# Performance work log

Measured on AMD Instinct MI355X. Metric: run time of the kernel, lower is better.

## Reference

```python
import jax, jax.numpy as jnp
import numpy as np

NUM_USERS = 100000
NUM_ITEMS = 50000
NUM_EDGES = 2000000
DIM = 64
NUM_REL = 5


def setup_inputs() -> dict:
    key = jax.random.key(0)
    k1, k2, k3, k4, k5, k6 = jax.random.split(key, 6)
    u_features = jax.random.normal(k1, (NUM_USERS, DIM), dtype=jnp.float32)
    i_features = jax.random.normal(k2, (NUM_ITEMS, DIM), dtype=jnp.float32)
    edge_user = jax.random.randint(k3, (NUM_EDGES,), 0, NUM_USERS, dtype=jnp.int64)
    edge_item = jax.random.randint(k4, (NUM_EDGES,), 0, NUM_ITEMS, dtype=jnp.int64)
    # per-relation Linear params, torch convention: y = x @ W[r].T + b[r]
    W = jax.random.normal(k5, (NUM_REL, DIM, DIM), dtype=jnp.float32) * (1.0 / np.sqrt(DIM))
    b = jax.random.normal(k6, (NUM_REL, DIM), dtype=jnp.float32) * 0.01
    return {"u_features": u_features, "i_features": i_features,
            "edge_user": edge_user, "edge_item": edge_item, "W": W, "b": b}


def reference(u_features, i_features, edge_user, edge_item, W, b):
    # gather edge endpoint features: [E, D]
    edge_u = u_features[edge_user]
    edge_i = i_features[edge_item]
    num_rel = W.shape[0]
    # per relation: sum((edge_u @ W[r].T + b[r]) * edge_i, axis=1) -> [E]
    # loop over small fixed relation count to avoid [E, R, D] intermediate
    cols = [jnp.sum((edge_u @ W[r].T + b[r]) * edge_i, axis=1)
            for r in range(num_rel)]
    return jnp.stack(cols, axis=1)  # [E, R]
```

## Files before the change

kernel.cpp:

```cpp
#include <hip/hip_runtime.h>
#include <stdint.h>

#define NREL 5
#define D 64
#define Q_BYTES 320
#define NT 21
#define NB 8
#define CHUNK 4096
#define EDGE_GRID 2048

typedef __attribute__((ext_vector_type(8))) short short8;
typedef __attribute__((ext_vector_type(4))) float f32x4;

static __device__ __forceinline__ short f2bf(float f) {
    uint32_t u = __float_as_uint(f);
    u += 0x7FFFu + ((u >> 16) & 1u);
    return (short)(u >> 16);
}

#if defined(__has_builtin)
#if __has_builtin(__builtin_amdgcn_sdot4)
#define HAVE_SDOT4 1
#endif
#endif
#ifdef HAVE_SDOT4
static __device__ __forceinline__ int SDOT4(uint32_t a, uint32_t b, int c) {
    return __builtin_amdgcn_sdot4((int)a, (int)b, c, false);
}
#else
static __device__ __forceinline__ int SDOT4(uint32_t a, uint32_t b, int c) {
    c += ((int)(a << 24) >> 24) * ((int)(b << 24) >> 24);
    c += ((int)(a << 16) >> 24) * ((int)(b << 16) >> 24);
    c += ((int)(a << 8) >> 24) * ((int)(b << 8) >> 24);
    c += ((int)a >> 24) * ((int)b >> 24);
    return c;
}
#endif

__global__ __launch_bounds__(256) void prep_kernel(
    const float* __restrict__ W, const float* __restrict__ bias_p, short* __restrict__ Wf,
    const float* __restrict__ uf, uint32_t* __restrict__ uq, float* __restrict__ uscale,
    int nUsers,
    const int* __restrict__ edge_user, const int* __restrict__ edge_item,
    int nE, int bucketDiv, int cap,
    int* __restrict__ totals, unsigned long long* __restrict__ sorted)
{
    __shared__ int cnt[NB];
    __shared__ int base[NB];
    const int nbW = (NT * 2 * 64 + 255) / 256;
    const int nbU = (nUsers * 16 + 255) / 256;
    int bid = blockIdx.x;

    if (bid < nbW) {
        const int tid = bid * 256 + threadIdx.x;
        if (tid >= NT * 2 * 64) return;
        const int lane = tid & 63;
        const int h = (tid >> 6) & 1;
        const int nt = tid >> 7;
        const int ln = lane & 15, quad = lane >> 4;
        const int n = nt * 16 + ln;
        uint32_t w[4];
#pragma unroll
        for (int p = 0; p < 4; ++p) {
            uint32_t lo = 0, hi = 0;
#pragma unroll
            for (int s = 0; s < 2; ++s) {
                const int j = p * 2 + s;
                const int d = h * 32 + quad * 8 + j;
                float v;
                if (nt < 20) v = W[(n >> 6) * (D * D) + d * D + (n & 63)];
                else         v = (ln < NREL) ? bias_p[ln * D + d] : 0.f;
                if (s == 0) lo = (uint16_t)f2bf(v); else hi = (uint16_t)f2bf(v);
            }
            w[p] = lo | (hi << 16);
        }
        *(uint4*)(Wf + (size_t)tid * 8) = make_uint4(w[0], w[1], w[2], w[3]);
        return;
    }
    bid -= nbW;

    if (bid < nbU) {
        const int gid = bid * 256 + threadIdx.x;
        const int row = gid >> 4;
        const int t = gid & 15;
        if (row >= nUsers) return;
        const float* rp = uf + (size_t)row * D;
        const float v0 = rp[t], v1 = rp[16 + t], v2 = rp[32 + t], v3 = rp[48 + t];
        float m = fmaxf(fmaxf(fabsf(v0), fabsf(v1)), fmaxf(fabsf(v2), fabsf(v3)));
        m = fmaxf(m, __shfl_xor(m, 1));
        m = fmaxf(m, __shfl_xor(m, 2));
        m = fmaxf(m, __shfl_xor(m, 4));
        m = fmaxf(m, __shfl_xor(m, 8));
        m = fmaxf(m, 1e-20f);
        const float qs = 127.0f / m;
        const int q0 = (int)rintf(v0 * qs);
        const int q1 = (int)rintf(v1 * qs);
        const int q2 = (int)rintf(v2 * qs);
        const int q3 = (int)rintf(v3 * qs);
        uq[(size_t)row * 16 + t] = ((uint32_t)(uint8_t)(int8_t)q0)
                                 | ((uint32_t)(uint8_t)(int8_t)q1 << 8)
                                 | ((uint32_t)(uint8_t)(int8_t)q2 << 16)
                                 | ((uint32_t)(uint8_t)(int8_t)q3 << 24);
        if (t == 0) uscale[row] = m * (1.0f / 127.0f);
        return;
    }
    bid -= nbU;

    if (threadIdx.x < NB) cnt[threadIdx.x] = 0;
    __syncthreads();

    const long start = (long)bid * CHUNK;
    unsigned long long pk[CHUNK / 256];
    unsigned long long bins = 0;
    unsigned long long accLo = 0, accHi = 0;
#pragma unroll
    for (int k = 0; k < CHUNK / 256; ++k) {
        const long e = start + k * 256 + threadIdx.x;
        const bool ok = (e < nE);
        int iu = 0, ii = 0;
        if (ok) { iu = edge_user[e]; ii = edge_item[e]; }
        pk[k] = ok ? ((unsigned long long)(uint32_t)iu
                    | ((unsigned long long)(uint32_t)ii << 17)
                    | ((unsigned long long)e << 33))
                   : ~0ull;
        const int bn = ok ? (ii / bucketDiv) : 0;
        bins |= (unsigned long long)bn << (k * 3);
        if (ok) {
            const unsigned long long one = 1ull << ((bn & 3) * 16);
            if (bn < 4) accLo += one; else accHi += one;
        }
    }
#pragma unroll
    for (int d = 1; d < 64; d <<= 1) {
        accLo += __shfl_xor(accLo, d);
        accHi += __shfl_xor(accHi, d);
    }
    if ((threadIdx.x & 63) == 0) {
#pragma unroll
        for (int f = 0; f < 4; ++f) {
            atomicAdd(&cnt[f],     (int)((accLo >> (f * 16)) & 0xFFFF));
            atomicAdd(&cnt[4 + f], (int)((accHi >> (f * 16)) & 0xFFFF));
        }
    }
    __syncthreads();
    if (threadIdx.x < NB) {
        const int c = cnt[threadIdx.x];
        base[threadIdx.x] = threadIdx.x * cap + atomicAdd(&totals[threadIdx.x], c);
        cnt[threadIdx.x] = 0;
    }
    __syncthreads();
#pragma unroll
    for (int k = 0; k < CHUNK / 256; ++k) {
        if (pk[k] != ~0ull) {
            const int bn = (int)((bins >> (k * 3)) & 7);
            const int r = atomicAdd(&cnt[bn], 1);
            sorted[base[bn] + r] = pk[k];
        }
    }
}

__global__ __launch_bounds__(256) void item_transform_kernel(
    const float* __restrict__ i_feat,
    const short* __restrict__ Wf,
    char* __restrict__ qrecs,
    float* __restrict__ sc,
    int nItems)
{
    const int lane = threadIdx.x & 63;
    const int wv = threadIdx.x >> 6;
    const int m0 = blockIdx.x * 64 + wv * 16;
    const int ln = lane & 15, quad = lane >> 4;

    int rowA = m0 + ln;
    if (rowA >= nItems) rowA = nItems - 1;
    const float* ap = i_feat + (size_t)rowA * D + quad * 8;
    short8 af[2];
#pragma unroll
    for (int h = 0; h < 2; ++h) {
        const float4 x = *(const float4*)(ap + h * 32);
        const float4 y = *(const float4*)(ap + h * 32 + 4);
        short8 a;
        a[0] = f2bf(x.x); a[1] = f2bf(x.y); a[2] = f2bf(x.z); a[3] = f2bf(x.w);
        a[4] = f2bf(y.x); a[5] = f2bf(y.y); a[6] = f2bf(y.z); a[7] = f2bf(y.w);
        af[h] = a;
    }

    f32x4 acc[NT];
#pragma unroll
    for (int nt = 0; nt < NT; ++nt) acc[nt] = (f32x4){0.f, 0.f, 0.f, 0.f};

#pragma unroll
    for (int nt = 0; nt < NT; ++nt) {
        const short8 b0 = *(const short8*)(Wf + ((size_t)(nt * 2 + 0) * 64 + lane) * 8);
        acc[nt] = __builtin_amdgcn_mfma_f32_16x16x32_bf16(af[0], b0, acc[nt], 0, 0, 0);
        const short8 b1 = *(const short8*)(Wf + ((size_t)(nt * 2 + 1) * 64 + lane) * 8);
        acc[nt] = __builtin_amdgcn_mfma_f32_16x16x32_bf16(af[1], b1, acc[nt], 0, 0, 0);
    }

#pragma unroll
    for (int g = 0; g < 4; ++g) {
        const int item = m0 + quad * 4 + g;
        const bool ok = (item < nItems);
        char* rec = qrecs + (size_t)item * Q_BYTES;
#pragma unroll
        for (int r = 0; r < NREL; ++r) {
            const float v0 = acc[4 * r + 0][g];
            const float v1 = acc[4 * r + 1][g];
            const float v2 = acc[4 * r + 2][g];
            const float v3 = acc[4 * r + 3][g];
            float m = fmaxf(fmaxf(fabsf(v0), fabsf(v1)), fmaxf(fabsf(v2), fabsf(v3)));
            m = fmaxf(m, __shfl_xor(m, 1));
            m = fmaxf(m, __shfl_xor(m, 2));
            m = fmaxf(m, __shfl_xor(m, 4));
            m = fmaxf(m, __shfl_xor(m, 8));
            m = fmaxf(m, 1e-20f);
            const float qs = 127.0f / m;
            const uint32_t pw = ((uint32_t)(uint8_t)(int8_t)(int)rintf(v0 * qs))
                              | ((uint32_t)(uint8_t)(int8_t)(int)rintf(v1 * qs) << 8)
                              | ((uint32_t)(uint8_t)(int8_t)(int)rintf(v2 * qs) << 16)
                              | ((uint32_t)(uint8_t)(int8_t)(int)rintf(v3 * qs) << 24);
            if (ok) {
                *(uint32_t*)(rec + r * D + ln * 4) = pw;
                if (ln == 0) sc[(size_t)item * 16 + 2 * r] = m * (1.0f / 127.0f);
            }
        }
        if (ok && ln < NREL) sc[(size_t)item * 16 + 2 * ln + 1] = acc[20][g];
    }
}

__global__ __launch_bounds__(256) void edge_kernel(
    const uint32_t* __restrict__ u_q,
    const float* __restrict__ u_scale,
    const unsigned long long* __restrict__ sorted,
    const int* __restrict__ totals, int cap,
    const char* __restrict__ qrecs,
    const float* __restrict__ sc,
    float* __restrict__ out)
{
    const int b = blockIdx.x & 7;
    const int seg = blockIdx.x >> 3;
    const int nSeg = gridDim.x >> 3;
    const int s0 = b * cap;
    const int s1 = s0 + totals[b];
    const int cnt = s1 - s0;
    const int per = (cnt + nSeg - 1) / nSeg;
    const int p0 = s0 + seg * per;
    const int p1 = min(p0 + per, s1);

    const int lane = threadIdx.x & 63;
    const int wv = threadIdx.x >> 6;
    const int es = lane >> 2;
    const int c = lane & 3;

    for (int q0 = p0 + wv * 16; q0 < p1; q0 += 64) {
        const int pos = q0 + es;
        if (pos < p1) {
            const unsigned long long pk = sorted[pos];
            const int iu = (int)(pk & 0x1FFFF);
            const int ii = (int)((pk >> 17) & 0xFFFF);
            const long e = (long)(pk >> 33);

            const uint4 uv = *(const uint4*)(u_q + (size_t)iu * 16 + c * 4);
            const char* rec = qrecs + (size_t)ii * Q_BYTES;

            int s[NREL];
#pragma unroll
            for (int r = 0; r < NREL; ++r) {
                const uint4 yv = *(const uint4*)(rec + r * D + c * 16);
                int t = SDOT4(uv.x, yv.x, 0);
                t = SDOT4(uv.y, yv.y, t);
                t = SDOT4(uv.z, yv.z, t);
                s[r] = SDOT4(uv.w, yv.w, t);
            }
#pragma unroll
            for (int r = 0; r < NREL; ++r) {
                s[r] += __shfl_xor(s[r], 1);
                s[r] += __shfl_xor(s[r], 2);
            }
            const float us = u_scale[iu];
            const float* scp = sc + (size_t)ii * 16;
            const float2 sb = *(const float2*)(scp + 2 * c);
            out[e * NREL + c] = fmaf((float)s[c], us * sb.x, sb.y);
            if (c == 0) {
                const float2 sb4 = *(const float2*)(scp + 8);
                out[e * NREL + 4] = fmaf((float)s[4], us * sb4.x, sb4.y);
            }
        }
    }
}

extern "C" void kernel_launch(void* const* d_in, const int* in_sizes, int n_in,
                              void* d_out, int out_size, void* d_ws, size_t ws_size,
                              hipStream_t stream) {
    const float* u_feat    = (const float*)d_in[0];
    const float* i_feat    = (const float*)d_in[1];
    const int*   edge_user = (const int*)d_in[2];
    const int*   edge_item = (const int*)d_in[3];
    const float* W         = (const float*)d_in[4];
    const float* b         = (const float*)d_in[5];
    float* out = (float*)d_out;

    const int nUsers = in_sizes[0] / D;
    const int nItems = in_sizes[1] / D;
    const int nE = in_sizes[2];
    const int bucketDiv = (nItems + NB - 1) / NB;
    const int nBlocksSort = (nE + CHUNK - 1) / CHUNK;
    const int cap = nE / NB + 32768;

    size_t off = 0;
    char* qrecs = (char*)d_ws;
    off += ((size_t)nItems * Q_BYTES + 255) & ~(size_t)255;
    float* sc = (float*)((char*)d_ws + off);
    off += ((size_t)nItems * 16 * sizeof(float) + 255) & ~(size_t)255;
    uint32_t* u_q = (uint32_t*)((char*)d_ws + off);
    off += ((size_t)nUsers * D + 255) & ~(size_t)255;
    float* u_scale = (float*)((char*)d_ws + off);
    off += ((size_t)nUsers * sizeof(float) + 255) & ~(size_t)255;
    short* Wf = (short*)((char*)d_ws + off);
    off += ((size_t)NT * 2 * 64 * 8 * sizeof(short) + 255) & ~(size_t)255;
    int* totals = (int*)((char*)d_ws + off);
    off += 256;
    unsigned long long* sorted = (unsigned long long*)((char*)d_ws + off);

    hipMemsetAsync(totals, 0, NB * sizeof(int), stream);

    const int nbW = (NT * 2 * 64 + 255) / 256;
    const int nbU = (nUsers * 16 + 255) / 256;
    prep_kernel<<<nbW + nbU + nBlocksSort, 256, 0, stream>>>(
        W, b, Wf, u_feat, u_q, u_scale, nUsers,
        edge_user, edge_item, nE, bucketDiv, cap, totals, sorted);
    item_transform_kernel<<<(nItems + 63) / 64, 256, 0, stream>>>(i_feat, Wf, qrecs, sc, nItems);
    edge_kernel<<<EDGE_GRID, 256, 0, stream>>>(u_q, u_scale, sorted, totals, cap,
                                               qrecs, sc, out);
}
```

Measured before the change: 259.1 us.

## Write edge results in sorted order, then unpermute to output order

The edge kernel now writes its per-edge results contiguously in bucket-sorted order with nontemporal stores, instead of scattering them to random output rows. The sort kernel also records a permutation, and a new unperm kernel gathers the results back to edge order with coalesced output writes. This is meant to cut the cost of scattered partial-line writes, at the price of an extra kernel launch, extra intermediate traffic (perm, resA, resB), and a dependence on workspace size. The bucket capacity slack is also reduced, which risks overflowing a bucket if bin counts are skewed.

```diff
diff --git a/kernel.cpp b/kernel.cpp
--- a/kernel.cpp
+++ b/kernel.cpp
@@ -43,7 +43,8 @@
     int nUsers,
     const int* __restrict__ edge_user, const int* __restrict__ edge_item,
     int nE, int bucketDiv, int cap,
-    int* __restrict__ totals, unsigned long long* __restrict__ sorted)
+    int* __restrict__ totals, unsigned long long* __restrict__ sorted,
+    int* __restrict__ perm, int twoPass)
 {
     __shared__ int cnt[NB];
     __shared__ int base[NB];
@@ -152,9 +153,12 @@
 #pragma unroll
     for (int k = 0; k < CHUNK / 256; ++k) {
         if (pk[k] != ~0ull) {
+            const long e = start + k * 256 + threadIdx.x;
             const int bn = (int)((bins >> (k * 3)) & 7);
             const int r = atomicAdd(&cnt[bn], 1);
-            sorted[base[bn] + r] = pk[k];
+            const int pos = base[bn] + r;
+            sorted[pos] = pk[k];
+            if (twoPass) perm[e] = pos;
         }
     }
 }
@@ -235,7 +239,10 @@
     const int* __restrict__ totals, int cap,
     const char* __restrict__ qrecs,
     const float* __restrict__ sc,
-    float* __restrict__ out)
+    float* __restrict__ resA,
+    float* __restrict__ resB,
+    float* __restrict__ out,
+    int twoPass)
 {
     const int b = blockIdx.x & 7;
     const int seg = blockIdx.x >> 3;
@@ -258,7 +265,6 @@
             const unsigned long long pk = sorted[pos];
             const int iu = (int)(pk & 0x1FFFF);
             const int ii = (int)((pk >> 17) & 0xFFFF);
-            const long e = (long)(pk >> 33);
 
             const uint4 uv = *(const uint4*)(u_q + (size_t)iu * 16 + c * 4);
             const char* rec = qrecs + (size_t)ii * Q_BYTES;
@@ -280,11 +286,41 @@
             const float us = u_scale[iu];
             const float* scp = sc + (size_t)ii * 16;
             const float2 sb = *(const float2*)(scp + 2 * c);
-            out[e * NREL + c] = fmaf((float)s[c], us * sb.x, sb.y);
+            const float v_c = fmaf((float)s[c], us * sb.x, sb.y);
+            float v_4 = 0.f;
             if (c == 0) {
                 const float2 sb4 = *(const float2*)(scp + 8);
-                out[e * NREL + 4] = fmaf((float)s[4], us * sb4.x, sb4.y);
-            }
+                v_4 = fmaf((float)s[4], us * sb4.x, sb4.y);
+            }
+            if (twoPass) {
+                __builtin_nontemporal_store(v_c, resA + (size_t)pos * 4 + c);
+                if (c == 0) __builtin_nontemporal_store(v_4, resB + pos);
+            } else {
+                const long e = (long)(pk >> 33);
+                out[e * NREL + c] = v_c;
+                if (c == 0) out[e * NREL + 4] = v_4;
+            }
+        }
+    }
+}
+
+__global__ __launch_bounds__(256) void unperm_kernel(
+    const int* __restrict__ perm,
+    const float4* __restrict__ resA,
+    const float* __restrict__ resB,
+    int nE,
+    float* __restrict__ out)
+{
+    const long start = (long)blockIdx.x * CHUNK;
+#pragma unroll
+    for (int k = 0; k < CHUNK / 256; ++k) {
+        const long e = start + k * 256 + threadIdx.x;
+        if (e < nE) {
+            const int p = perm[e];
+            const float4 a = resA[p];
+            const float b5 = resB[p];
+            float* op = out + e * NREL;
+            op[0] = a.x; op[1] = a.y; op[2] = a.z; op[3] = a.w; op[4] = b5;
         }
     }
 }
@@ -305,7 +341,7 @@
     const int nE = in_sizes[2];
     const int bucketDiv = (nItems + NB - 1) / NB;
     const int nBlocksSort = (nE + CHUNK - 1) / CHUNK;
-    const int cap = nE / NB + 32768;
+    const int cap = nE / NB + 4096;
 
     size_t off = 0;
     char* qrecs = (char*)d_ws;
@@ -321,6 +357,14 @@
     int* totals = (int*)((char*)d_ws + off);
     off += 256;
     unsigned long long* sorted = (unsigned long long*)((char*)d_ws + off);
+    off += ((size_t)NB * cap * sizeof(unsigned long long) + 255) & ~(size_t)255;
+    int* perm = (int*)((char*)d_ws + off);
+    size_t off2 = off + (((size_t)nE * sizeof(int) + 255) & ~(size_t)255);
+    float* resA = (float*)((char*)d_ws + off2);
+    off2 += ((size_t)NB * cap * 4 * sizeof(float) + 255) & ~(size_t)255;
+    float* resB = (float*)((char*)d_ws + off2);
+    off2 += ((size_t)NB * cap * sizeof(float) + 255) & ~(size_t)255;
+    const int twoPass = (ws_size >= off2) ? 1 : 0;
 
     hipMemsetAsync(totals, 0, NB * sizeof(int), stream);
 
@@ -328,8 +372,10 @@
     const int nbU = (nUsers * 16 + 255) / 256;
     prep_kernel<<<nbW + nbU + nBlocksSort, 256, 0, stream>>>(
         W, b, Wf, u_feat, u_q, u_scale, nUsers,
-        edge_user, edge_item, nE, bucketDiv, cap, totals, sorted);
+        edge_user, edge_item, nE, bucketDiv, cap, totals, sorted, perm, twoPass);
     item_transform_kernel<<<(nItems + 63) / 64, 256, 0, stream>>>(i_feat, Wf, qrecs, sc, nItems);
     edge_kernel<<<EDGE_GRID, 256, 0, stream>>>(u_q, u_scale, sorted, totals, cap,
-                                               qrecs, sc, out);
-}
+                                               qrecs, sc, resA, resB, out, twoPass);
+    if (twoPass)
+        unperm_kernel<<<nBlocksSort, 256, 0, stream>>>(perm, (const float4*)resA, resB, nE, out);
+}
```

New measurement: 258.6 us. No clear change (-0.2%).

## Compact sort keys, write sorted-order results, and unpermute outputs in separate pass

Applied to the files above, without the earlier changes.

The sort records shrink from 64-bit to 32-bit by storing the bucket-local item index and dropping the edge id. A 16-bit per-edge permutation and per-block bucket bases are recorded instead. The edge kernel now writes results contiguously in sorted order with nontemporal stores, replacing scattered 20-byte output writes, and a new unperm kernel gathers them back into edge order. Item transform is merged into the user-quant/sort kernel, while W prep moves to its own tiny kernel. The cost is an extra kernel launch plus extra intermediate read/write traffic, and the bucket slack is reduced.

```diff
diff --git a/kernel.cpp b/kernel.cpp
--- a/kernel.cpp
+++ b/kernel.cpp
@@ -37,205 +37,206 @@
 }
 #endif
 
-__global__ __launch_bounds__(256) void prep_kernel(
-    const float* __restrict__ W, const float* __restrict__ bias_p, short* __restrict__ Wf,
-    const float* __restrict__ uf, uint32_t* __restrict__ uq, float* __restrict__ uscale,
-    int nUsers,
+__global__ __launch_bounds__(256) void wprep_kernel(
+    const float* __restrict__ W, const float* __restrict__ bias_p, short* __restrict__ Wf)
+{
+    const int tid = blockIdx.x * 256 + threadIdx.x;
+    if (tid >= NT * 2 * 64) return;
+    const int lane = tid & 63;
+    const int h = (tid >> 6) & 1;
+    const int nt = tid >> 7;
+    const int ln = lane & 15, quad = lane >> 4;
+    const int n = nt * 16 + ln;
+    uint32_t w[4];
+#pragma unroll
+    for (int p = 0; p < 4; ++p) {
+        uint32_t lo = 0, hi = 0;
+#pragma unroll
+        for (int s = 0; s < 2; ++s) {
+            const int j = p * 2 + s;
+            const int d = h * 32 + quad * 8 + j;
+            float v;
+            if (nt < 20) v = W[(n >> 6) * (D * D) + d * D + (n & 63)];
+            else         v = (ln < NREL) ? bias_p[ln * D + d] : 0.f;
+            if (s == 0) lo = (uint16_t)f2bf(v); else hi = (uint16_t)f2bf(v);
+        }
+        w[p] = lo | (hi << 16);
+    }
+    *(uint4*)(Wf + (size_t)tid * 8) = make_uint4(w[0], w[1], w[2], w[3]);
+}
+
+__global__ __launch_bounds__(256) void fused_kernel(
+    const float* __restrict__ i_feat, const short* __restrict__ Wf,
+    char* __restrict__ qrecs, float* __restrict__ sc, int nItems,
+    const float* __restrict__ uf, uint32_t* __restrict__ uq,
+    float* __restrict__ uscale, int nUsers,
     const int* __restrict__ edge_user, const int* __restrict__ edge_item,
     int nE, int bucketDiv, int cap,
-    int* __restrict__ totals, unsigned long long* __restrict__ sorted)
+    int* __restrict__ totals, uint32_t* __restrict__ sorted,
+    uint16_t* __restrict__ perm, int* __restrict__ blockBase)
 {
     __shared__ int cnt[NB];
     __shared__ int base[NB];
-    const int nbW = (NT * 2 * 64 + 255) / 256;
-    const int nbU = (nUsers * 16 + 255) / 256;
+    const int nbI = (nItems + 63) / 64;
+    const int nbS = (nE + CHUNK - 1) / CHUNK;
     int bid = blockIdx.x;
 
-    if (bid < nbW) {
-        const int tid = bid * 256 + threadIdx.x;
-        if (tid >= NT * 2 * 64) return;
-        const int lane = tid & 63;
-        const int h = (tid >> 6) & 1;
-        const int nt = tid >> 7;
+    if (bid < nbI) {
+        const int lane = threadIdx.x & 63;
+        const int wv = threadIdx.x >> 6;
+        const int m0 = bid * 64 + wv * 16;
         const int ln = lane & 15, quad = lane >> 4;
-        const int n = nt * 16 + ln;
-        uint32_t w[4];
-#pragma unroll
-        for (int p = 0; p < 4; ++p) {
-            uint32_t lo = 0, hi = 0;
-#pragma unroll
-            for (int s = 0; s < 2; ++s) {
-                const int j = p * 2 + s;
-                const int d = h * 32 + quad * 8 + j;
-                float v;
-                if (nt < 20) v = W[(n >> 6) * (D * D) + d * D + (n & 63)];
-                else         v = (ln < NREL) ? bias_p[ln * D + d] : 0.f;
-                if (s == 0) lo = (uint16_t)f2bf(v); else hi = (uint16_t)f2bf(v);
-            }
-            w[p] = lo | (hi << 16);
-        }
-        *(uint4*)(Wf + (size_t)tid * 8) = make_uint4(w[0], w[1], w[2], w[3]);
+
+        int rowA = m0 + ln;
+        if (rowA >= nItems) rowA = nItems - 1;
+        const float* ap = i_feat + (size_t)rowA * D + quad * 8;
+        short8 af[2];
+#pragma unroll
+        for (int h = 0; h < 2; ++h) {
+            const float4 x = *(const float4*)(ap + h * 32);
+            const float4 y = *(const float4*)(ap + h * 32 + 4);
+            short8 a;
+            a[0] = f2bf(x.x); a[1] = f2bf(x.y); a[2] = f2bf(x.z); a[3] = f2bf(x.w);
+            a[4] = f2bf(y.x); a[5] = f2bf(y.y); a[6] = f2bf(y.z); a[7] = f2bf(y.w);
+            af[h] = a;
+        }
+
+        f32x4 acc[NT];
+#pragma unroll
+        for (int nt = 0; nt < NT; ++nt) acc[nt] = (f32x4){0.f, 0.f, 0.f, 0.f};
+
+#pragma unroll
+        for (int nt = 0; nt < NT; ++nt) {
+            const short8 b0 = *(const short8*)(Wf + ((size_t)(nt * 2 + 0) * 64 + lane) * 8);
+            acc[nt] = __builtin_amdgcn_mfma_f32_16x16x32_bf16(af[0], b0, acc[nt], 0, 0, 0);
+            const short8 b1 = *(const short8*)(Wf + ((size_t)(nt * 2 + 1) * 64 + lane) * 8);
+            acc[nt] = __builtin_amdgcn_mfma_f32_16x16x32_bf16(af[1], b1, acc[nt], 0, 0, 0);
+        }
+
+#pragma unroll
+        for (int g = 0; g < 4; ++g) {
+            const int item = m0 + quad * 4 + g;
+            const bool ok = (item < nItems);
+            char* rec = qrecs + (size_t)item * Q_BYTES;
+#pragma unroll
+            for (int r = 0; r < NREL; ++r) {
+                const float v0 = acc[4 * r + 0][g];
+                const float v1 = acc[4 * r + 1][g];
+                const float v2 = acc[4 * r + 2][g];
+                const float v3 = acc[4 * r + 3][g];
+                float m = fmaxf(fmaxf(fabsf(v0), fabsf(v1)), fmaxf(fabsf(v2), fabsf(v3)));
+                m = fmaxf(m, __shfl_xor(m, 1));
+                m = fmaxf(m, __shfl_xor(m, 2));
+                m = fmaxf(m, __shfl_xor(m, 4));
+                m = fmaxf(m, __shfl_xor(m, 8));
+                m = fmaxf(m, 1e-20f);
+                const float qs = 127.0f / m;
+                const uint32_t pw = ((uint32_t)(uint8_t)(int8_t)(int)rintf(v0 * qs))
+                                  | ((uint32_t)(uint8_t)(int8_t)(int)rintf(v1 * qs) << 8)
+                                  | ((uint32_t)(uint8_t)(int8_t)(int)rintf(v2 * qs) << 16)
+                                  | ((uint32_t)(uint8_t)(int8_t)(int)rintf(v3 * qs) << 24);
+                if (ok) {
+                    *(uint32_t*)(rec + r * D + ln * 4) = pw;
+                    if (ln == 0) sc[(size_t)item * 16 + 2 * r] = m * (1.0f / 127.0f);
+                }
+            }
+            if (ok && ln < NREL) sc[(size_t)item * 16 + 2 * ln + 1] = acc[20][g];
+        }
         return;
     }
-    bid -= nbW;
-
-    if (bid < nbU) {
-        const int gid = bid * 256 + threadIdx.x;
-        const int row = gid >> 4;
-        const int t = gid & 15;
-        if (row >= nUsers) return;
-        const float* rp = uf + (size_t)row * D;
-        const float v0 = rp[t], v1 = rp[16 + t], v2 = rp[32 + t], v3 = rp[48 + t];
-        float m = fmaxf(fmaxf(fabsf(v0), fabsf(v1)), fmaxf(fabsf(v2), fabsf(v3)));
-        m = fmaxf(m, __shfl_xor(m, 1));
-        m = fmaxf(m, __shfl_xor(m, 2));
-        m = fmaxf(m, __shfl_xor(m, 4));
-        m = fmaxf(m, __shfl_xor(m, 8));
-        m = fmaxf(m, 1e-20f);
-        const float qs = 127.0f / m;
-        const int q0 = (int)rintf(v0 * qs);
-        const int q1 = (int)rintf(v1 * qs);
-        const int q2 = (int)rintf(v2 * qs);
-        const int q3 = (int)rintf(v3 * qs);
-        uq[(size_t)row * 16 + t] = ((uint32_t)(uint8_t)(int8_t)q0)
-                                 | ((uint32_t)(uint8_t)(int8_t)q1 << 8)
-                                 | ((uint32_t)(uint8_t)(int8_t)q2 << 16)
-                                 | ((uint32_t)(uint8_t)(int8_t)q3 << 24);
-        if (t == 0) uscale[row] = m * (1.0f / 127.0f);
+    bid -= nbI;
+
+    if (bid < nbS) {
+        if (threadIdx.x < NB) cnt[threadIdx.x] = 0;
+        __syncthreads();
+
+        const long start = (long)bid * CHUNK;
+        uint32_t pk[CHUNK / 256];
+        unsigned long long bins = 0;
+        unsigned long long accLo = 0, accHi = 0;
+#pragma unroll
+        for (int k = 0; k < CHUNK / 256; ++k) {
+            const long e = start + k * 256 + threadIdx.x;
+            const bool ok = (e < nE);
+            int iu = 0, ii = 0;
+            if (ok) { iu = edge_user[e]; ii = edge_item[e]; }
+            const int bn = ok ? (ii / bucketDiv) : 0;
+            const int iiL = ii - bn * bucketDiv;
+            pk[k] = ok ? ((uint32_t)iu | ((uint32_t)iiL << 17)) : 0xFFFFFFFFu;
+            bins |= (unsigned long long)bn << (k * 3);
+            if (ok) {
+                const unsigned long long one = 1ull << ((bn & 3) * 16);
+                if (bn < 4) accLo += one; else accHi += one;
+            }
+        }
+#pragma unroll
+        for (int d = 1; d < 64; d <<= 1) {
+            accLo += __shfl_xor(accLo, d);
+            accHi += __shfl_xor(accHi, d);
+        }
+        if ((threadIdx.x & 63) == 0) {
+#pragma unroll
+            for (int f = 0; f < 4; ++f) {
+                atomicAdd(&cnt[f],     (int)((accLo >> (f * 16)) & 0xFFFF));
+                atomicAdd(&cnt[4 + f], (int)((accHi >> (f * 16)) & 0xFFFF));
+            }
+        }
+        __syncthreads();
+        if (threadIdx.x < NB) {
+            const int c = cnt[threadIdx.x];
+            const int bs = threadIdx.x * cap + atomicAdd(&totals[threadIdx.x], c);
+            base[threadIdx.x] = bs;
+            blockBase[bid * NB + threadIdx.x] = bs;
+            cnt[threadIdx.x] = 0;
+        }
+        __syncthreads();
+#pragma unroll
+        for (int k = 0; k < CHUNK / 256; ++k) {
+            if (pk[k] != 0xFFFFFFFFu) {
+                const long e = start + k * 256 + threadIdx.x;
+                const int bn = (int)((bins >> (k * 3)) & 7);
+                const int r = atomicAdd(&cnt[bn], 1);
+                sorted[base[bn] + r] = pk[k];
+                perm[e] = (uint16_t)((bn << 12) | r);
+            }
+        }
         return;
     }
-    bid -= nbU;
-
-    if (threadIdx.x < NB) cnt[threadIdx.x] = 0;
-    __syncthreads();
-
-    const long start = (long)bid * CHUNK;
-    unsigned long long pk[CHUNK / 256];
-    unsigned long long bins = 0;
-    unsigned long long accLo = 0, accHi = 0;
-#pragma unroll
-    for (int k = 0; k < CHUNK / 256; ++k) {
-        const long e = start + k * 256 + threadIdx.x;
-        const bool ok = (e < nE);
-        int iu = 0, ii = 0;
-        if (ok) { iu = edge_user[e]; ii = edge_item[e]; }
-        pk[k] = ok ? ((unsigned long long)(uint32_t)iu
-                    | ((unsigned long long)(uint32_t)ii << 17)
-                    | ((unsigned long long)e << 33))
-                   : ~0ull;
-        const int bn = ok ? (ii / bucketDiv) : 0;
-        bins |= (unsigned long long)bn << (k * 3);
-        if (ok) {
-            const unsigned long long one = 1ull << ((bn & 3) * 16);
-            if (bn < 4) accLo += one; else accHi += one;
-        }
-    }
-#pragma unroll
-    for (int d = 1; d < 64; d <<= 1) {
-        accLo += __shfl_xor(accLo, d);
-        accHi += __shfl_xor(accHi, d);
-    }
-    if ((threadIdx.x & 63) == 0) {
-#pragma unroll
-        for (int f = 0; f < 4; ++f) {
-            atomicAdd(&cnt[f],     (int)((accLo >> (f * 16)) & 0xFFFF));
-            atomicAdd(&cnt[4 + f], (int)((accHi >> (f * 16)) & 0xFFFF));
-        }
-    }
-    __syncthreads();
-    if (threadIdx.x < NB) {
-        const int c = cnt[threadIdx.x];
-        base[threadIdx.x] = threadIdx.x * cap + atomicAdd(&totals[threadIdx.x], c);
-        cnt[threadIdx.x] = 0;
-    }
-    __syncthreads();
-#pragma unroll
-    for (int k = 0; k < CHUNK / 256; ++k) {
-        if (pk[k] != ~0ull) {
-            const int bn = (int)((bins >> (k * 3)) & 7);
-            const int r = atomicAdd(&cnt[bn], 1);
-            sorted[base[bn] + r] = pk[k];
-        }
-    }
-}
-
-__global__ __launch_bounds__(256) void item_transform_kernel(
-    const float* __restrict__ i_feat,
-    const short* __restrict__ Wf,
-    char* __restrict__ qrecs,
-    float* __restrict__ sc,
-    int nItems)
-{
-    const int lane = threadIdx.x & 63;
-    const int wv = threadIdx.x >> 6;
-    const int m0 = blockIdx.x * 64 + wv * 16;
-    const int ln = lane & 15, quad = lane >> 4;
-
-    int rowA = m0 + ln;
-    if (rowA >= nItems) rowA = nItems - 1;
-    const float* ap = i_feat + (size_t)rowA * D + quad * 8;
-    short8 af[2];
-#pragma unroll
-    for (int h = 0; h < 2; ++h) {
-        const float4 x = *(const float4*)(ap + h * 32);
-        const float4 y = *(const float4*)(ap + h * 32 + 4);
-        short8 a;
-        a[0] = f2bf(x.x); a[1] = f2bf(x.y); a[2] = f2bf(x.z); a[3] = f2bf(x.w);
-        a[4] = f2bf(y.x); a[5] = f2bf(y.y); a[6] = f2bf(y.z); a[7] = f2bf(y.w);
-        af[h] = a;
-    }
-
-    f32x4 acc[NT];
-#pragma unroll
-    for (int nt = 0; nt < NT; ++nt) acc[nt] = (f32x4){0.f, 0.f, 0.f, 0.f};
-
-#pragma unroll
-    for (int nt = 0; nt < NT; ++nt) {
-        const short8 b0 = *(const short8*)(Wf + ((size_t)(nt * 2 + 0) * 64 + lane) * 8);
-        acc[nt] = __builtin_amdgcn_mfma_f32_16x16x32_bf16(af[0], b0, acc[nt], 0, 0, 0);
-        const short8 b1 = *(const short8*)(Wf + ((size_t)(nt * 2 + 1) * 64 + lane) * 8);
-        acc[nt] = __builtin_amdgcn_mfma_f32_16x16x32_bf16(af[1], b1, acc[nt], 0, 0, 0);
-    }
-
-#pragma unroll
-    for (int g = 0; g < 4; ++g) {
-        const int item = m0 + quad * 4 + g;
-        const bool ok = (item < nItems);
-        char* rec = qrecs + (size_t)item * Q_BYTES;
-#pragma unroll
-        for (int r = 0; r < NREL; ++r) {
-            const float v0 = acc[4 * r + 0][g];
-            const float v1 = acc[4 * r + 1][g];
-            const float v2 = acc[4 * r + 2][g];
-            const float v3 = acc[4 * r + 3][g];
-            float m = fmaxf(fmaxf(fabsf(v0), fabsf(v1)), fmaxf(fabsf(v2), fabsf(v3)));
-            m = fmaxf(m, __shfl_xor(m, 1));
-            m = fmaxf(m, __shfl_xor(m, 2));
-            m = fmaxf(m, __shfl_xor(m, 4));
-            m = fmaxf(m, __shfl_xor(m, 8));
-            m = fmaxf(m, 1e-20f);
-            const float qs = 127.0f / m;
-            const uint32_t pw = ((uint32_t)(uint8_t)(int8_t)(int)rintf(v0 * qs))
-                              | ((uint32_t)(uint8_t)(int8_t)(int)rintf(v1 * qs) << 8)
-                              | ((uint32_t)(uint8_t)(int8_t)(int)rintf(v2 * qs) << 16)
-                              | ((uint32_t)(uint8_t)(int8_t)(int)rintf(v3 * qs) << 24);
-            if (ok) {
-                *(uint32_t*)(rec + r * D + ln * 4) = pw;
-                if (ln == 0) sc[(size_t)item * 16 + 2 * r] = m * (1.0f / 127.0f);
-            }
-        }
-        if (ok && ln < NREL) sc[(size_t)item * 16 + 2 * ln + 1] = acc[20][g];
-    }
+    bid -= nbS;
+
+    const int gid = bid * 256 + threadIdx.x;
+    const int row = gid >> 4;
+    const int t = gid & 15;
+    if (row >= nUsers) return;
+    const float* rp = uf + (size_t)row * D;
+    const float v0 = rp[t], v1 = rp[16 + t], v2 = rp[32 + t], v3 = rp[48 + t];
+    float m = fmaxf(fmaxf(fabsf(v0), fabsf(v1)), fmaxf(fabsf(v2), fabsf(v3)));
+    m = fmaxf(m, __shfl_xor(m, 1));
+    m = fmaxf(m, __shfl_xor(m, 2));
+    m = fmaxf(m, __shfl_xor(m, 4));
+    m = fmaxf(m, __shfl_xor(m, 8));
+    m = fmaxf(m, 1e-20f);
+    const float qs = 127.0f / m;
+    const int q0 = (int)rintf(v0 * qs);
+    const int q1 = (int)rintf(v1 * qs);
+    const int q2 = (int)rintf(v2 * qs);
+    const int q3 = (int)rintf(v3 * qs);
+    uq[(size_t)row * 16 + t] = ((uint32_t)(uint8_t)(int8_t)q0)
+                             | ((uint32_t)(uint8_t)(int8_t)q1 << 8)
+                             | ((uint32_t)(uint8_t)(int8_t)q2 << 16)
+                             | ((uint32_t)(uint8_t)(int8_t)q3 << 24);
+    if (t == 0) uscale[row] = m * (1.0f / 127.0f);
 }
 
 __global__ __launch_bounds__(256) void edge_kernel(
     const uint32_t* __restrict__ u_q,
     const float* __restrict__ u_scale,
-    const unsigned long long* __restrict__ sorted,
-    const int* __restrict__ totals, int cap,
+    const uint32_t* __restrict__ sorted,
+    const int* __restrict__ totals, int cap, int bucketDiv,
     const char* __restrict__ qrecs,
     const float* __restrict__ sc,
-    float* __restrict__ out)
+    float* __restrict__ resA,
+    float* __restrict__ resB)
 {
     const int b = blockIdx.x & 7;
     const int seg = blockIdx.x >> 3;
@@ -251,14 +252,14 @@
     const int wv = threadIdx.x >> 6;
     const int es = lane >> 2;
     const int c = lane & 3;
+    const int itemBase = b * bucketDiv;
 
     for (int q0 = p0 + wv * 16; q0 < p1; q0 += 64) {
         const int pos = q0 + es;
         if (pos < p1) {
-            const unsigned long long pk = sorted[pos];
+            const uint32_t pk = sorted[pos];
             const int iu = (int)(pk & 0x1FFFF);
-            const int ii = (int)((pk >> 17) & 0xFFFF);
-            const long e = (long)(pk >> 33);
+            const int ii = itemBase + (int)(pk >> 17);
 
             const uint4 uv = *(const uint4*)(u_q + (size_t)iu * 16 + c * 4);
             const char* rec = qrecs + (size_t)ii * Q_BYTES;
@@ -280,11 +281,39 @@
             const float us = u_scale[iu];
             const float* scp = sc + (size_t)ii * 16;
             const float2 sb = *(const float2*)(scp + 2 * c);
-            out[e * NREL + c] = fmaf((float)s[c], us * sb.x, sb.y);
+            __builtin_nontemporal_store(fmaf((float)s[c], us * sb.x, sb.y),
+                                        resA + (size_t)pos * 4 + c);
             if (c == 0) {
                 const float2 sb4 = *(const float2*)(scp + 8);
-                out[e * NREL + 4] = fmaf((float)s[4], us * sb4.x, sb4.y);
-            }
+                __builtin_nontemporal_store(fmaf((float)s[4], us * sb4.x, sb4.y),
+                                            resB + pos);
+            }
+        }
+    }
+}
+
+__global__ __launch_bounds__(256) void unperm_kernel(
+    const uint16_t* __restrict__ perm,
+    const int* __restrict__ blockBase,
+    const float4* __restrict__ resA,
+    const float* __restrict__ resB,
+    int nE,
+    float* __restrict__ out)
+{
+    __shared__ int bb[NB];
+    if (threadIdx.x < NB) bb[threadIdx.x] = blockBase[blockIdx.x * NB + threadIdx.x];
+    __syncthreads();
+    const long start = (long)blockIdx.x * CHUNK;
+#pragma unroll
+    for (int k = 0; k < CHUNK / 256; ++k) {
+        const long e = start + k * 256 + threadIdx.x;
+        if (e < nE) {
+            const int pr = perm[e];
+            const int p = bb[pr >> 12] + (pr & 0xFFF);
+            const float4 a = resA[p];
+            const float b5 = resB[p];
+            float* op = out + e * NREL;
+            op[0] = a.x; op[1] = a.y; op[2] = a.z; op[3] = a.w; op[4] = b5;
         }
     }
 }
@@ -305,7 +334,7 @@
     const int nE = in_sizes[2];
     const int bucketDiv = (nItems + NB - 1) / NB;
     const int nBlocksSort = (nE + CHUNK - 1) / CHUNK;
-    const int cap = nE / NB + 32768;
+    const int cap = nE / NB + 4096;
 
     size_t off = 0;
     char* qrecs = (char*)d_ws;
@@ -320,16 +349,31 @@
     off += ((size_t)NT * 2 * 64 * 8 * sizeof(short) + 255) & ~(size_t)255;
     int* totals = (int*)((char*)d_ws + off);
     off += 256;
-    unsigned long long* sorted = (unsigned long long*)((char*)d_ws + off);
+    int* blockBase = (int*)((char*)d_ws + off);
+    off += ((size_t)nBlocksSort * NB * sizeof(int) + 255) & ~(size_t)255;
+    uint32_t* sorted = (uint32_t*)((char*)d_ws + off);
+    off += ((size_t)NB * cap * sizeof(uint32_t) + 255) & ~(size_t)255;
+    uint16_t* perm = (uint16_t*)((char*)d_ws + off);
+    off += ((size_t)nE * sizeof(uint16_t) + 255) & ~(size_t)255;
+    float* resA = (float*)((char*)d_ws + off);
+    off += ((size_t)NB * cap * 4 * sizeof(float) + 255) & ~(size_t)255;
+    float* resB = (float*)((char*)d_ws + off);
+    off += ((size_t)NB * cap * sizeof(float) + 255) & ~(size_t)255;
 
     hipMemsetAsync(totals, 0, NB * sizeof(int), stream);
 
-    const int nbW = (NT * 2 * 64 + 255) / 256;
+    wprep_kernel<<<(NT * 2 * 64 + 255) / 256, 256, 0, stream>>>(W, b, Wf);
+
+    const int nbI = (nItems + 63) / 64;
     const int nbU = (nUsers * 16 + 255) / 256;
-    prep_kernel<<<nbW + nbU + nBlocksSort, 256, 0, stream>>>(
-        W, b, Wf, u_feat, u_q, u_scale, nUsers,
-        edge_user, edge_item, nE, bucketDiv, cap, totals, sorted);
-    item_transform_kernel<<<(nItems + 63) / 64, 256, 0, stream>>>(i_feat, Wf, qrecs, sc, nItems);
-    edge_kernel<<<EDGE_GRID, 256, 0, stream>>>(u_q, u_scale, sorted, totals, cap,
-                                               qrecs, sc, out);
-}
+    fused_kernel<<<nbI + nBlocksSort + nbU, 256, 0, stream>>>(
+        i_feat, Wf, qrecs, sc, nItems,
+        u_feat, u_q, u_scale, nUsers,
+        edge_user, edge_item, nE, bucketDiv, cap,
+        totals, sorted, perm, blockBase);
+
+    edge_kernel<<<EDGE_GRID, 256, 0, stream>>>(u_q, u_scale, sorted, totals, cap, bucketDiv,
+                                               qrecs, sc, resA, resB);
+    unperm_kernel<<<nBlocksSort, 256, 0, stream>>>(perm, blockBase,
+                                                   (const float4*)resA, resB, nE, out);
+}
```

New measurement: 240.9 us. -7.0%, faster.
